# Kernel tuning notes

Measured on AMD Instinct MI355X. Metric: run time of the kernel, lower is better.

Reference implementation:

```python
import jax, jax.numpy as jnp
import numpy as np

EPS = 1e-12  # tf.nn.l2_normalize epsilon


def _l2norm(x, axis):
    # tf.nn.l2_normalize: x / sqrt(max(sum(x^2), eps))
    return x * jax.lax.rsqrt(jnp.maximum(jnp.sum(x * x, axis=axis, keepdims=True), EPS))


def setup_inputs() -> dict:
    key = jax.random.key(0)
    k0, k1, k2, k3 = jax.random.split(key, 4)
    B, L, E, C, NG = 128, 1024, 300, 20, 55
    return {
        "x_emb": jax.random.normal(k0, (B, L, E), jnp.float32),
        "x_mask": jnp.ones((B, L), jnp.float32),            # mask_seq = tf.ones(...) in call()
        "W_class": jax.random.normal(k1, (B, C, E), jnp.float32),
        "conv_w": jax.random.normal(k2, (NG, C, C), jnp.float32) * 0.05,  # [width, in=C, out=C]
        "conv_b": jnp.zeros((C,), jnp.float32),
        "W_dis": jax.random.normal(k3, (C, E), jnp.float32) * 0.05,       # 20 per-class 0-layer discriminators
        "b_dis": jnp.zeros((C,), jnp.float32),
    }


def reference(x_emb, x_mask, W_class, conv_w, conv_b, W_dis, b_dis):
    # --- att_emb_ngram_encoder_cnn ---
    x0 = x_emb * x_mask[..., None]                       # b s e (masked word embeddings)
    xn = _l2norm(x0, 2)                                  # b s e
    wn = _l2norm(W_class, 2)                             # b c e (normalize over embed dim)
    G = jnp.einsum('bse,bce->bsc', xn, wn)               # cosine label-word attention, b s c
    # ngram conv smoothing over sequence, SAME padding, relu
    att = jax.lax.conv_general_dilated(
        G, conv_w, window_strides=(1,), padding='SAME',
        dimension_numbers=('NWC', 'WIO', 'NWC')) + conv_b  # b s c
    att = jax.nn.relu(att)
    # partial (masked) softmax over sequence dim
    ew = jnp.exp(att) * x_mask[..., None]                # b s c
    beta = ew / jnp.sum(ew, axis=1, keepdims=True)       # b s c
    # per-class attentive pooling of (unmasked) word embeddings: H_enc b e c
    H = jnp.einsum('bse,bsc->bec', x_emb, beta)
    # --- 20 per-class 0-layer discriminators (dropout is identity at inference) ---
    logits = jnp.einsum('bec,ce->bc', H, W_dis) + b_dis  # b c
    return logits
```

## Files before the change

kernel.cpp:

```cpp
#include <hip/hip_runtime.h>
#include <math.h>

#define B 128
#define L 1024
#define E 300
#define C 20

#define OFF_WNT 0
#define OFF_WDT 768000
#define OFF_SWC 774000
#define OFF_G   796400
#define OFF_D   3417840
#define OFF_S   6039280
#define OFF_T   6041840

__global__ __launch_bounds__(256) void prep_kernel(
    const float* __restrict__ Wc, const float* __restrict__ convw,
    const float* __restrict__ wdis,
    float* __restrict__ wnT, float* __restrict__ wdT,
    float* __restrict__ swc, float* __restrict__ ST)
{
  int t = threadIdx.x;
  int gid = blockIdx.x * 256 + t;

  if (gid < 2 * B * C) ST[gid] = 0.f;

  if (gid < 55 * C * C) {
    int w  = gid / (C * C);
    int r  = gid % (C * C);
    int ci = r / C, co = r % C;
    swc[(((size_t)ci * 4 + co / 5) * 14 + (w >> 2)) * 20 + (co % 5) * 4 + (w & 3)] = convw[gid];
  }
  if (gid < C * C) {
    int ci = gid / C, co = gid % C;
    swc[(((size_t)ci * 4 + co / 5) * 14 + 13) * 20 + (co % 5) * 4 + 3] = 0.f;
  }
  if (gid < 6000) {
    int og = gid / 1500, rem = gid % 1500;
    int kq = rem / 20, i = rem % 20;
    int co = og * 5 + i / 4, q = i & 3;
    wdT[gid] = wdis[(size_t)co * E + kq * 4 + q];
  }

  int row = blockIdx.x * 4 + (t >> 6);
  int ln  = t & 63;
  if (row < B * C) {
    int bb = row / C, c = row % C;
    const float* src = Wc + (size_t)row * E;
    float v[5];
    float ss = 0.f;
    #pragma unroll
    for (int k = 0; k < 5; ++k) {
      int e = ln + 64 * k;
      v[k] = (e < E) ? src[e] : 0.f;
      ss += v[k] * v[k];
    }
    #pragma unroll
    for (int off = 32; off; off >>= 1) ss += __shfl_xor(ss, off, 64);
    float r = rsqrtf(fmaxf(ss, 1e-12f));
    float* dst = wnT + ((size_t)bb * 4 + c / 5) * 1500;
    int cosub = (c % 5) * 4;
    #pragma unroll
    for (int k = 0; k < 5; ++k) {
      int e = ln + 64 * k;
      if (e < E) dst[(e >> 2) * 20 + cosub + (e & 3)] = v[k] * r;
    }
  }
}

__global__ __launch_bounds__(512, 4) void gemm_kernel(
    const float* __restrict__ x, const float* __restrict__ wnT,
    const float* __restrict__ wdT, float* __restrict__ Gt, float* __restrict__ Dt)
{
  __shared__ float xs[32 * 256];

  int t  = threadIdx.x;
  int ln = t & 63;
  int wid   = __builtin_amdgcn_readfirstlane(t >> 6);
  int og    = wid & 3;
  int shalf = wid >> 2;
  int b  = blockIdx.y;
  int s0 = blockIdx.x * 256;
  int sl = shalf * 128 + ln * 2;

  const float* wnbase = wnT + ((size_t)b * 4 + og) * 1500;
  const float* wdbase = wdT + (size_t)og * 1500;

  float accG[5][2], accD[5][2];
  #pragma unroll
  for (int c = 0; c < 5; ++c) {
    accG[c][0] = accG[c][1] = 0.f;
    accD[c][0] = accD[c][1] = 0.f;
  }
  float ssq0 = 0.f, ssq1 = 0.f;

  for (int chunk = 0; chunk < 10; ++chunk) {
    int k0 = chunk * 32;
    int krem = E - k0; if (krem > 32) krem = 32;

    const float* xb = x + ((size_t)b * L + s0) * E + k0;
    #pragma unroll
    for (int it = 0; it < 4; ++it) {
      int idx = it * 512 + t;
      int row = idx >> 3, col = idx & 7;
      if (col * 4 < krem) {
        float4 f = *(const float4*)(xb + (size_t)row * E + col * 4);
        int r = row ^ ((col & 3) * 8);
        xs[(col * 4 + 0) * 256 + r] = f.x;
        xs[(col * 4 + 1) * 256 + r] = f.y;
        xs[(col * 4 + 2) * 256 + r] = f.z;
        xs[(col * 4 + 3) * 256 + r] = f.w;
      }
    }
    __syncthreads();

    int nq = krem >> 2;
    bool own_ssq = ((chunk & 3) == og);
    #pragma unroll
    for (int kq = 0; kq < 8; ++kq) {
      if (kq < nq) {
        const float* wn_p = wnbase + (chunk * 8 + kq) * 20;
        const float* wd_p = wdbase + (chunk * 8 + kq) * 20;
        float wG[20], wD[20];
        #pragma unroll
        for (int i = 0; i < 20; ++i) { wG[i] = wn_p[i]; wD[i] = wd_p[i]; }
        int rbase = sl ^ ((kq & 3) * 8);
        float2 xk[4];
        #pragma unroll
        for (int q = 0; q < 4; ++q)
          xk[q] = *(const float2*)&xs[(kq * 4 + q) * 256 + rbase];
        if (own_ssq) {
          #pragma unroll
          for (int q = 0; q < 4; ++q) {
            ssq0 = fmaf(xk[q].x, xk[q].x, ssq0);
            ssq1 = fmaf(xk[q].y, xk[q].y, ssq1);
          }
        }
        #pragma unroll
        for (int q = 0; q < 4; ++q) {
          #pragma unroll
          for (int c = 0; c < 5; ++c) {
            float wg = wG[c * 4 + q];
            float wv = wD[c * 4 + q];
            accG[c][0] = fmaf(xk[q].x, wg, accG[c][0]);
            accG[c][1] = fmaf(xk[q].y, wg, accG[c][1]);
            accD[c][0] = fmaf(xk[q].x, wv, accD[c][0]);
            accD[c][1] = fmaf(xk[q].y, wv, accD[c][1]);
          }
        }
      }
    }
    __syncthreads();
  }

  *(float2*)&xs[og * 256 + sl] = make_float2(ssq0, ssq1);
  __syncthreads();
  float2 p0 = *(const float2*)&xs[      sl];
  float2 p1 = *(const float2*)&xs[256 + sl];
  float2 p2 = *(const float2*)&xs[512 + sl];
  float2 p3 = *(const float2*)&xs[768 + sl];
  float rinv0 = rsqrtf(fmaxf(p0.x + p1.x + p2.x + p3.x, 1e-12f));
  float rinv1 = rsqrtf(fmaxf(p0.y + p1.y + p2.y + p3.y, 1e-12f));

  int s = s0 + sl;
  #pragma unroll
  for (int c = 0; c < 5; ++c) {
    float2 g = { accG[c][0] * rinv0, accG[c][1] * rinv1 };
    *(float2*)&Gt[((size_t)b * C + og * 5 + c) * L + s] = g;
    float2 d = { accD[c][0], accD[c][1] };
    *(float2*)&Dt[((size_t)b * C + og * 5 + c) * L + s] = d;
  }
}

#define GP 312
__global__ __launch_bounds__(512, 4) void conv_kernel(
    const float* __restrict__ Gt, const float* __restrict__ Dt,
    const float* __restrict__ swc, const float* __restrict__ convb,
    float* __restrict__ S, float* __restrict__ T)
{
  __shared__ float g_lds[C * GP];

  int t  = threadIdx.x;
  int ln = t & 63;
  int wid = __builtin_amdgcn_readfirstlane(t >> 6);
  int og  = wid & 3;
  int cih = wid >> 2;
  int b  = blockIdx.y;
  int s0 = blockIdx.x * 256;

  for (int c = 0; c < C; ++c)
    for (int h = t; h < GP; h += 512) {
      int s = s0 - 27 + h;
      g_lds[c * GP + h] = (s >= 0 && s < L) ? Gt[((size_t)b * C + c) * L + s] : 0.f;
    }
  __syncthreads();

  float acc[4][5];
  #pragma unroll
  for (int j = 0; j < 4; ++j)
    #pragma unroll
    for (int c = 0; c < 5; ++c) acc[j][c] = 0.f;

  for (int ci = cih * 10; ci < cih * 10 + 10; ++ci) {
    const float* gl = &g_lds[ci * GP + ln * 4];
    const float* wp = swc + ((size_t)ci * 4 + og) * 280;
    float4 g0 = *(const float4*)gl;
    #pragma unroll
    for (int wq = 0; wq < 14; ++wq) {
      float4 g1 = *(const float4*)(gl + wq * 4 + 4);
      float w[20];
      #pragma unroll
      for (int i = 0; i < 20; ++i) w[i] = wp[wq * 20 + i];
      float ga[7] = {g0.x, g0.y, g0.z, g0.w, g1.x, g1.y, g1.z};
      #pragma unroll
      for (int q = 0; q < 4; ++q) {
        #pragma unroll
        for (int j = 0; j < 4; ++j) {
          float gv = ga[q + j];
          #pragma unroll
          for (int c = 0; c < 5; ++c)
            acc[j][c] = fmaf(gv, w[c * 4 + q], acc[j][c]);
        }
      }
      g0 = g1;
    }
  }

  __syncthreads();
  float* scr = g_lds;
  int pr = (og * 64 + ln) * 21;
  if (cih == 1) {
    #pragma unroll
    for (int j = 0; j < 4; ++j)
      #pragma unroll
      for (int c = 0; c < 5; ++c) scr[pr + j * 5 + c] = acc[j][c];
  }
  __syncthreads();

  if (cih == 0) {
    #pragma unroll
    for (int j = 0; j < 4; ++j)
      #pragma unroll
      for (int c = 0; c < 5; ++c) acc[j][c] += scr[pr + j * 5 + c];

    float se[5], st_[5];
    int s = s0 + ln * 4;
    #pragma unroll
    for (int c = 0; c < 5; ++c) {
      float cb = convb[og * 5 + c];
      float4 d4 = *(const float4*)&Dt[((size_t)b * C + og * 5 + c) * L + s];
      const float* df = (const float*)&d4;
      float e0 = 0.f, e1 = 0.f;
      #pragma unroll
      for (int j = 0; j < 4; ++j) {
        float a = acc[j][c] + cb;
        float e = expf(fmaxf(a, 0.f));
        e0 += e;
        e1 += e * df[j];
      }
      se[c] = e0; st_[c] = e1;
    }
    #pragma unroll
    for (int c = 0; c < 5; ++c) {
      #pragma unroll
      for (int off = 32; off; off >>= 1) {
        se[c]  += __shfl_xor(se[c],  off, 64);
        st_[c] += __shfl_xor(st_[c], off, 64);
      }
    }
    if (ln == 0) {
      #pragma unroll
      for (int c = 0; c < 5; ++c) {
        atomicAdd(&S[b * C + og * 5 + c], se[c]);
        atomicAdd(&T[b * C + og * 5 + c], st_[c]);
      }
    }
  }
}

__global__ __launch_bounds__(256) void fin_kernel(
    const float* __restrict__ S, const float* __restrict__ T,
    const float* __restrict__ bdis, float* __restrict__ out)
{
  int i = blockIdx.x * 256 + threadIdx.x;
  if (i < B * C) out[i] = T[i] / S[i] + bdis[i % C];
}

extern "C" void kernel_launch(void* const* d_in, const int* in_sizes, int n_in,
                              void* d_out, int out_size, void* d_ws, size_t ws_size,
                              hipStream_t stream) {
  const float* x_emb = (const float*)d_in[0];
  const float* Wc    = (const float*)d_in[2];
  const float* convw = (const float*)d_in[3];
  const float* convb = (const float*)d_in[4];
  const float* wdis  = (const float*)d_in[5];
  const float* bdis  = (const float*)d_in[6];

  float* ws  = (float*)d_ws;
  float* wnT = ws + OFF_WNT;
  float* wdT = ws + OFF_WDT;
  float* swc = ws + OFF_SWC;
  float* Gt  = ws + OFF_G;
  float* Dt  = ws + OFF_D;
  float* S   = ws + OFF_S;
  float* T   = ws + OFF_T;
  float* out = (float*)d_out;

  prep_kernel<<<640, 256, 0, stream>>>(Wc, convw, wdis, wnT, wdT, swc, S);
  gemm_kernel<<<dim3(L / 256, B), 512, 0, stream>>>(x_emb, wnT, wdT, Gt, Dt);
  conv_kernel<<<dim3(L / 256, B), 512, 0, stream>>>(Gt, Dt, swc, convb, S, T);
  fin_kernel<<<10, 256, 0, stream>>>(S, T, bdis, out);
}
```

Baseline: 332.8 us.

## Double-buffer x tiles in LDS with register prefetch in gemm kernel

```diff
diff --git a/kernel.cpp b/kernel.cpp
--- a/kernel.cpp
+++ b/kernel.cpp
@@ -72,7 +72,7 @@
     const float* __restrict__ x, const float* __restrict__ wnT,
     const float* __restrict__ wdT, float* __restrict__ Gt, float* __restrict__ Dt)
 {
-  __shared__ float xs[32 * 256];
+  __shared__ float xs[2][32 * 256];
 
   int t  = threadIdx.x;
   int ln = t & 63;
@@ -85,6 +85,12 @@
 
   const float* wnbase = wnT + ((size_t)b * 4 + og) * 1500;
   const float* wdbase = wdT + (size_t)og * 1500;
+  const float* xb = x + ((size_t)b * L + s0) * E;
+
+  int col   = t & 7;
+  int row0  = t >> 3;
+  int rsw   = row0 ^ ((col & 3) * 8);
+  const float* xcol = xb + (size_t)row0 * E + col * 4;
 
   float accG[5][2], accD[5][2];
   #pragma unroll
@@ -94,27 +100,42 @@
   }
   float ssq0 = 0.f, ssq1 = 0.f;
 
+  {
+    float4 f0 = *(const float4*)(xcol);
+    float4 f1 = *(const float4*)(xcol +  64 * E);
+    float4 f2 = *(const float4*)(xcol + 128 * E);
+    float4 f3 = *(const float4*)(xcol + 192 * E);
+    float* bp = &xs[0][0];
+    #pragma unroll
+    for (int j = 0; j < 4; ++j) {
+      float v0 = ((const float*)&f0)[j], v1 = ((const float*)&f1)[j];
+      float v2 = ((const float*)&f2)[j], v3 = ((const float*)&f3)[j];
+      bp[(col * 4 + j) * 256 + rsw      ] = v0;
+      bp[(col * 4 + j) * 256 + rsw +  64] = v1;
+      bp[(col * 4 + j) * 256 + rsw + 128] = v2;
+      bp[(col * 4 + j) * 256 + rsw + 192] = v3;
+    }
+  }
+  __syncthreads();
+
   for (int chunk = 0; chunk < 10; ++chunk) {
-    int k0 = chunk * 32;
-    int krem = E - k0; if (krem > 32) krem = 32;
-
-    const float* xb = x + ((size_t)b * L + s0) * E + k0;
-    #pragma unroll
-    for (int it = 0; it < 4; ++it) {
-      int idx = it * 512 + t;
-      int row = idx >> 3, col = idx & 7;
-      if (col * 4 < krem) {
-        float4 f = *(const float4*)(xb + (size_t)row * E + col * 4);
-        int r = row ^ ((col & 3) * 8);
-        xs[(col * 4 + 0) * 256 + r] = f.x;
-        xs[(col * 4 + 1) * 256 + r] = f.y;
-        xs[(col * 4 + 2) * 256 + r] = f.z;
-        xs[(col * 4 + 3) * 256 + r] = f.w;
-      }
-    }
-    __syncthreads();
-
+    int cur = chunk & 1;
+    int krem = E - chunk * 32; if (krem > 32) krem = 32;
     int nq = krem >> 2;
+
+    float4 f0, f1, f2, f3;
+    bool have_next = (chunk < 9);
+    int krem_n = E - (chunk + 1) * 32; if (krem_n > 32) krem_n = 32;
+    bool ld = have_next && (col * 4 < krem_n);
+    if (ld) {
+      const float* p = xcol + (chunk + 1) * 32;
+      f0 = *(const float4*)(p);
+      f1 = *(const float4*)(p +  64 * E);
+      f2 = *(const float4*)(p + 128 * E);
+      f3 = *(const float4*)(p + 192 * E);
+    }
+
+    const float* bp = &xs[cur][0];
     bool own_ssq = ((chunk & 3) == og);
     #pragma unroll
     for (int kq = 0; kq < 8; ++kq) {
@@ -128,7 +149,7 @@
         float2 xk[4];
         #pragma unroll
         for (int q = 0; q < 4; ++q)
-          xk[q] = *(const float2*)&xs[(kq * 4 + q) * 256 + rbase];
+          xk[q] = *(const float2*)&bp[(kq * 4 + q) * 256 + rbase];
         if (own_ssq) {
           #pragma unroll
           for (int q = 0; q < 4; ++q) {
@@ -150,15 +171,28 @@
         }
       }
     }
+
+    if (ld) {
+      float* wb = &xs[cur ^ 1][0];
+      #pragma unroll
+      for (int j = 0; j < 4; ++j) {
+        float v0 = ((const float*)&f0)[j], v1 = ((const float*)&f1)[j];
+        float v2 = ((const float*)&f2)[j], v3 = ((const float*)&f3)[j];
+        wb[(col * 4 + j) * 256 + rsw      ] = v0;
+        wb[(col * 4 + j) * 256 + rsw +  64] = v1;
+        wb[(col * 4 + j) * 256 + rsw + 128] = v2;
+        wb[(col * 4 + j) * 256 + rsw + 192] = v3;
+      }
+    }
     __syncthreads();
   }
 
-  *(float2*)&xs[og * 256 + sl] = make_float2(ssq0, ssq1);
-  __syncthreads();
-  float2 p0 = *(const float2*)&xs[      sl];
-  float2 p1 = *(const float2*)&xs[256 + sl];
-  float2 p2 = *(const float2*)&xs[512 + sl];
-  float2 p3 = *(const float2*)&xs[768 + sl];
+  *(float2*)&xs[0][og * 256 + sl] = make_float2(ssq0, ssq1);
+  __syncthreads();
+  float2 p0 = *(const float2*)&xs[0][      sl];
+  float2 p1 = *(const float2*)&xs[0][256 + sl];
+  float2 p2 = *(const float2*)&xs[0][512 + sl];
+  float2 p3 = *(const float2*)&xs[0][768 + sl];
   float rinv0 = rsqrtf(fmaxf(p0.x + p1.x + p2.x + p3.x, 1e-12f));
   float rinv1 = rsqrtf(fmaxf(p0.y + p1.y + p2.y + p3.y, 1e-12f));
 
```

Result: slower. 348.6 us (+4.7%).

## Shrink gemm tiles to 64 rows and register-prefetch next x chunk

Applied to the files above, without the earlier changes.

```diff
diff --git a/kernel.cpp b/kernel.cpp
--- a/kernel.cpp
+++ b/kernel.cpp
@@ -68,52 +68,51 @@
   }
 }
 
-__global__ __launch_bounds__(512, 4) void gemm_kernel(
+__global__ __launch_bounds__(256, 8) void gemm_kernel(
     const float* __restrict__ x, const float* __restrict__ wnT,
     const float* __restrict__ wdT, float* __restrict__ Gt, float* __restrict__ Dt)
 {
-  __shared__ float xs[32 * 256];
+  __shared__ float xs[32 * 64];
 
   int t  = threadIdx.x;
   int ln = t & 63;
-  int wid   = __builtin_amdgcn_readfirstlane(t >> 6);
-  int og    = wid & 3;
-  int shalf = wid >> 2;
+  int og = __builtin_amdgcn_readfirstlane(t >> 6);
   int b  = blockIdx.y;
-  int s0 = blockIdx.x * 256;
-  int sl = shalf * 128 + ln * 2;
+  int s0 = blockIdx.x * 64;
 
   const float* wnbase = wnT + ((size_t)b * 4 + og) * 1500;
   const float* wdbase = wdT + (size_t)og * 1500;
 
-  float accG[5][2], accD[5][2];
-  #pragma unroll
-  for (int c = 0; c < 5; ++c) {
-    accG[c][0] = accG[c][1] = 0.f;
-    accD[c][0] = accD[c][1] = 0.f;
-  }
-  float ssq0 = 0.f, ssq1 = 0.f;
+  int col = t & 7;
+  int r0  = (t >> 3) * 2;
+  int sw  = r0 ^ (col * 4);
+  const float* xcol = x + ((size_t)b * L + s0 + r0) * E + col * 4;
+
+  float accG[5] = {0.f, 0.f, 0.f, 0.f, 0.f};
+  float accD[5] = {0.f, 0.f, 0.f, 0.f, 0.f};
+  float ssq = 0.f;
+
+  {
+    float4 f0 = *(const float4*)(xcol);
+    float4 f1 = *(const float4*)(xcol + E);
+    #pragma unroll
+    for (int j = 0; j < 4; ++j)
+      *(float2*)&xs[(col * 4 + j) * 64 + sw] =
+          make_float2(((const float*)&f0)[j], ((const float*)&f1)[j]);
+  }
+  __syncthreads();
 
   for (int chunk = 0; chunk < 10; ++chunk) {
-    int k0 = chunk * 32;
-    int krem = E - k0; if (krem > 32) krem = 32;
-
-    const float* xb = x + ((size_t)b * L + s0) * E + k0;
-    #pragma unroll
-    for (int it = 0; it < 4; ++it) {
-      int idx = it * 512 + t;
-      int row = idx >> 3, col = idx & 7;
-      if (col * 4 < krem) {
-        float4 f = *(const float4*)(xb + (size_t)row * E + col * 4);
-        int r = row ^ ((col & 3) * 8);
-        xs[(col * 4 + 0) * 256 + r] = f.x;
-        xs[(col * 4 + 1) * 256 + r] = f.y;
-        xs[(col * 4 + 2) * 256 + r] = f.z;
-        xs[(col * 4 + 3) * 256 + r] = f.w;
-      }
-    }
-    __syncthreads();
-
+    float4 f0, f1;
+    int krem_n = E - (chunk + 1) * 32; if (krem_n > 32) krem_n = 32;
+    bool ld = (chunk < 9) && (col * 4 < krem_n);
+    if (ld) {
+      const float* p = xcol + (chunk + 1) * 32;
+      f0 = *(const float4*)(p);
+      f1 = *(const float4*)(p + E);
+    }
+
+    int krem = E - chunk * 32; if (krem > 32) krem = 32;
     int nq = krem >> 2;
     bool own_ssq = ((chunk & 3) == og);
     #pragma unroll
@@ -124,51 +123,45 @@
         float wG[20], wD[20];
         #pragma unroll
         for (int i = 0; i < 20; ++i) { wG[i] = wn_p[i]; wD[i] = wd_p[i]; }
-        int rbase = sl ^ ((kq & 3) * 8);
-        float2 xk[4];
+        const float* xr = &xs[kq * 4 * 64 + (ln ^ (kq * 4))];
+        float xv[4];
         #pragma unroll
-        for (int q = 0; q < 4; ++q)
-          xk[q] = *(const float2*)&xs[(kq * 4 + q) * 256 + rbase];
+        for (int q = 0; q < 4; ++q) xv[q] = xr[q * 64];
         if (own_ssq) {
           #pragma unroll
-          for (int q = 0; q < 4; ++q) {
-            ssq0 = fmaf(xk[q].x, xk[q].x, ssq0);
-            ssq1 = fmaf(xk[q].y, xk[q].y, ssq1);
-          }
+          for (int q = 0; q < 4; ++q) ssq = fmaf(xv[q], xv[q], ssq);
         }
         #pragma unroll
         for (int q = 0; q < 4; ++q) {
           #pragma unroll
           for (int c = 0; c < 5; ++c) {
-            float wg = wG[c * 4 + q];
-            float wv = wD[c * 4 + q];
-            accG[c][0] = fmaf(xk[q].x, wg, accG[c][0]);
-            accG[c][1] = fmaf(xk[q].y, wg, accG[c][1]);
-            accD[c][0] = fmaf(xk[q].x, wv, accD[c][0]);
-            accD[c][1] = fmaf(xk[q].y, wv, accD[c][1]);
+            accG[c] = fmaf(xv[q], wG[c * 4 + q], accG[c]);
+            accD[c] = fmaf(xv[q], wD[c * 4 + q], accD[c]);
           }
         }
       }
     }
     __syncthreads();
-  }
-
-  *(float2*)&xs[og * 256 + sl] = make_float2(ssq0, ssq1);
-  __syncthreads();
-  float2 p0 = *(const float2*)&xs[      sl];
-  float2 p1 = *(const float2*)&xs[256 + sl];
-  float2 p2 = *(const float2*)&xs[512 + sl];
-  float2 p3 = *(const float2*)&xs[768 + sl];
-  float rinv0 = rsqrtf(fmaxf(p0.x + p1.x + p2.x + p3.x, 1e-12f));
-  float rinv1 = rsqrtf(fmaxf(p0.y + p1.y + p2.y + p3.y, 1e-12f));
-
-  int s = s0 + sl;
+
+    if (ld) {
+      #pragma unroll
+      for (int j = 0; j < 4; ++j)
+        *(float2*)&xs[(col * 4 + j) * 64 + sw] =
+            make_float2(((const float*)&f0)[j], ((const float*)&f1)[j]);
+    }
+    __syncthreads();
+  }
+
+  xs[og * 64 + ln] = ssq;
+  __syncthreads();
+  float rinv = rsqrtf(fmaxf(xs[ln] + xs[64 + ln] + xs[128 + ln] + xs[192 + ln],
+                            1e-12f));
+
+  int s = s0 + ln;
   #pragma unroll
   for (int c = 0; c < 5; ++c) {
-    float2 g = { accG[c][0] * rinv0, accG[c][1] * rinv1 };
-    *(float2*)&Gt[((size_t)b * C + og * 5 + c) * L + s] = g;
-    float2 d = { accD[c][0], accD[c][1] };
-    *(float2*)&Dt[((size_t)b * C + og * 5 + c) * L + s] = d;
+    Gt[((size_t)b * C + og * 5 + c) * L + s] = accG[c] * rinv;
+    Dt[((size_t)b * C + og * 5 + c) * L + s] = accD[c];
   }
 }
 
@@ -307,7 +300,7 @@
   float* out = (float*)d_out;
 
   prep_kernel<<<640, 256, 0, stream>>>(Wc, convw, wdis, wnT, wdT, swc, S);
-  gemm_kernel<<<dim3(L / 256, B), 512, 0, stream>>>(x_emb, wnT, wdT, Gt, Dt);
+  gemm_kernel<<<dim3(L / 64, B), 256, 0, stream>>>(x_emb, wnT, wdT, Gt, Dt);
   conv_kernel<<<dim3(L / 256, B), 512, 0, stream>>>(Gt, Dt, swc, convb, S, T);
   fin_kernel<<<10, 256, 0, stream>>>(S, T, bdis, out);
 }
```

Result: slower. 350.2 us (+5.2%).
